# Performance work log

Hardware: AMD Instinct MI355X
Metric: run time of the kernel (lower is better)

## Reference

```python
import jax, jax.numpy as jnp
import numpy as np

STRIDES = (8, 16, 32)
IMG = 608
NC = 80
A = 3
IGNORE = 0.5
ANCHORS = np.array([[12, 16], [19, 36], [40, 28], [36, 75], [76, 55], [72, 146],
                    [142, 110], [192, 243], [459, 401]], np.float32)
ANCH_MASKS = ((0, 1, 2), (3, 4, 5), (6, 7, 8))
B, NL, NVALID = 16, 60, 45


def setup_inputs():
    key = jax.random.key(0)
    ks = jax.random.split(key, 8)
    inp = {}
    for i, s in enumerate(STRIDES):
        f = IMG // s
        inp[f"xin{i}"] = jax.random.normal(ks[i], (B, A * (5 + NC), f, f), jnp.float32)
    cx = jax.random.uniform(ks[3], (B, NL), minval=40.0, maxval=568.0)
    cy = jax.random.uniform(ks[4], (B, NL), minval=40.0, maxval=568.0)
    w = jax.random.uniform(ks[5], (B, NL), minval=8.0, maxval=120.0)
    h = jax.random.uniform(ks[6], (B, NL), minval=8.0, maxval=120.0)
    cls = jax.random.randint(ks[7], (B, NL), 0, NC).astype(jnp.float32)
    labels = jnp.stack([cx - w / 2, cy - h / 2, cx + w / 2, cy + h / 2, cls], -1)
    mask = (jnp.arange(NL) < NVALID)[None, :, None]
    inp["labels"] = jnp.where(mask, labels, 0.0)
    return inp


def _iou_cxcywh(p, t):  # p:[M,4] cx,cy,w,h; t:[N,4] -> [M,N]
    tl = jnp.maximum(p[:, None, :2] - p[:, None, 2:] / 2, t[None, :, :2] - t[None, :, 2:] / 2)
    br = jnp.minimum(p[:, None, :2] + p[:, None, 2:] / 2, t[None, :, :2] + t[None, :, 2:] / 2)
    ap = p[:, 2] * p[:, 3]
    at = t[:, 2] * t[:, 3]
    en = jnp.all(tl < br, -1)
    ai = jnp.prod(br - tl, -1) * en
    return ai / (ap[:, None] + at[None, :] - ai)


def _bce(p, t, w=None):
    # torch F.binary_cross_entropy with log clamped; clamp p instead (grad-safe, value-identical here)
    lp = jnp.log(jnp.maximum(p, 1e-12))
    l1p = jnp.log1p(-jnp.minimum(p, 1.0 - 1e-7))
    l = -(t * lp + (1.0 - t) * l1p)
    if w is not None:
        l = l * w
    return l.sum()


def _scale_loss(raw, labels, sid):
    stride = STRIDES[sid]
    f = IMG // stride
    n_ch = 5 + NC
    all_g = ANCHORS / stride  # [9,2] anchors in grid units
    m_anch = jnp.asarray(all_g[list(ANCH_MASKS[sid])])  # [3,2]
    b = raw.shape[0]
    out = raw.reshape(b, A, n_ch, f, f).transpose(0, 1, 3, 4, 2)  # [B,A,f,f,n_ch]
    xy = jax.nn.sigmoid(out[..., :2])
    wh = out[..., 2:4]
    obj = jax.nn.sigmoid(out[..., 4])
    clsp = jax.nn.sigmoid(out[..., 5:])

    gx = jnp.arange(f, dtype=jnp.float32)
    pred = jnp.stack([xy[..., 0] + gx[None, None, None, :],
                      xy[..., 1] + gx[None, None, :, None],
                      jnp.exp(wh[..., 0]) * m_anch[:, 0][None, :, None, None],
                      jnp.exp(wh[..., 1]) * m_anch[:, 1][None, :, None, None]], -1)

    valid = labels.sum(2) > 0  # [B,N]
    tx = (labels[..., 0] + labels[..., 2]) / (2 * stride)
    ty = (labels[..., 1] + labels[..., 3]) / (2 * stride)
    tw = (labels[..., 2] - labels[..., 0]) / stride
    th = (labels[..., 3] - labels[..., 1]) / stride
    ii = tx.astype(jnp.int32)
    jj = ty.astype(jnp.int32)

    # anchor-target IoU: both boxes anchored at origin -> closed form
    rw = jnp.asarray(all_g[:, 0])
    rh = jnp.asarray(all_g[:, 1])
    mw = jnp.minimum(tw[..., None], rw)
    mh = jnp.minimum(th[..., None], rh)
    inter = mw * mh * ((mw > 0) & (mh > 0))
    aiou = inter / (tw[..., None] * th[..., None] + rw * rh - inter)  # [B,N,9]
    best_all = jnp.argmax(aiou, -1)
    best_n = best_all % 3
    use = valid & (best_all // 3 == sid)

    # ignore mask from pred-vs-truth IoU
    tbox = jnp.stack([tx, ty, tw, th], -1)  # [B,N,4]
    ious = jax.vmap(_iou_cxcywh)(pred.reshape(b, -1, 4), tbox)  # [B,A*f*f,N]
    ious = ious * valid[:, None, :]
    obj_mask = (ious.max(-1).reshape(b, A, f, f) <= IGNORE).astype(jnp.float32)

    bb = jnp.broadcast_to(jnp.arange(b)[:, None], (b, labels.shape[1])).ravel()
    aa = best_n.ravel()
    jjs = jnp.where(use, jj, f).ravel()  # out-of-bounds index -> update dropped
    iis = ii.ravel()

    def scat(v):
        return jnp.zeros((b, A, f, f), jnp.float32).at[bb, aa, jjs, iis].set(v.ravel(), mode='drop')

    t0 = scat(tx - ii.astype(jnp.float32))
    t1 = scat(ty - jj.astype(jnp.float32))
    t2 = scat(jnp.log(tw / m_anch[best_n, 0] + 1e-16))
    t3 = scat(jnp.log(th / m_anch[best_n, 1] + 1e-16))
    t4 = scat(jnp.ones_like(tx))
    m = scat(jnp.ones_like(tx))
    sc = scat(jnp.sqrt(2.0 - tw * th / (f * f)))
    tcls = jnp.zeros((b, A, f, f, NC), jnp.float32).at[
        bb, aa, jjs, iis, labels[..., 4].astype(jnp.int32).ravel()].set(1.0, mode='drop')
    obj_mask = obj_mask.at[bb, aa, jjs, iis].set(1.0, mode='drop')

    m1 = m[..., None]
    sc1 = sc[..., None]
    o_xy = xy * m1
    g_xy = jnp.stack([t0, t1], -1) * m1
    o_wh = wh * m1 * sc1
    g_wh = jnp.stack([t2, t3], -1) * m1 * sc1
    o_ob = obj * obj_mask
    g_ob = t4 * obj_mask
    o_cl = clsp * m1
    g_cl = tcls * m1

    l_xy = _bce(o_xy, g_xy, (sc * sc)[..., None])
    l_wh = 0.5 * jnp.sum((o_wh - g_wh) ** 2)
    l_ob = _bce(o_ob, g_ob)
    l_cl = _bce(o_cl, g_cl)
    fo = jnp.concatenate([o_xy, o_wh, o_ob[..., None], o_cl], -1)
    ft = jnp.concatenate([g_xy, g_wh, g_ob[..., None], g_cl], -1)
    l2 = jnp.sum((fo - ft) ** 2)
    return jnp.stack([l_xy, l_wh, l_ob, l_cl, l2])


def reference(xin0, xin1, xin2, labels):
    parts = (_scale_loss(xin0, labels, 0) + _scale_loss(xin1, labels, 1)
             + _scale_loss(xin2, labels, 2))
    l_xy, l_wh, l_ob, l_cl, l2 = parts
    return jnp.stack([l_xy + l_wh + l_ob + l_cl, l_xy, l_wh, l_ob, l_cl, l2])
```

## Files before the change

### kernel.cpp

```cpp
#include <hip/hip_runtime.h>

#define BB 16
#define NL 60
#define NA 3
#define NC 80

#define NBX0C 17
#define NBX1C 5
#define NBX2C 2
#define NBXC  (NBX0C+NBX1C+NBX2C)
#define NBX   (NBXC+3)
#define NBLKT (NBX*BB)

__device__ __constant__ float d_AW[9] = {12.f,19.f,40.f,36.f,76.f,72.f,142.f,192.f,459.f};
__device__ __constant__ float d_AH[9] = {16.f,36.f,28.f,75.f,55.f,146.f,110.f,243.f,401.f};

__device__ __forceinline__ float sig_pos(float v){ return __fdividef(1.0f, 1.0f + __expf(-v)); }
__device__ __forceinline__ float sig_neg(float v){ return __fdividef(1.0f, 1.0f + __expf(v)); }
__device__ __forceinline__ float bcef(float p, float t){
    float lp  = __logf(fmaxf(p, 1e-12f));
    float l1p = __logf(1.0f - fminf(p, 1.0f - 1e-7f));
    return -(t*lp + (1.0f - t)*l1p);
}

template<int SID>
__device__ __forceinline__ bool cell_load(const float* __restrict__ raw, int xoff, int b, int tid,
        int &a, int &rembase, int &nc,
        float (&cx)[4], float (&cy)[4], float (&cw)[4], float (&ch)[4], float (&co)[4])
{
    constexpr int F  = (SID==0)?76:(SID==1)?38:19;
    constexpr int FF = F*F;
    int t = xoff*256 + tid;
    if (SID < 2){
        constexpr int NT = 3*FF/4;
        if (t >= NT) return false;
        a = t / (FF/4);
        rembase = 4*t - a*FF;
        nc = 4;
        const float* base = raw + ((size_t)(b*(NA*85) + a*85))*FF + rembase;
        float4 q0 = *reinterpret_cast<const float4*>(base);
        float4 q1 = *reinterpret_cast<const float4*>(base +   (size_t)FF);
        float4 q2 = *reinterpret_cast<const float4*>(base + 2*(size_t)FF);
        float4 q3 = *reinterpret_cast<const float4*>(base + 3*(size_t)FF);
        float4 q4 = *reinterpret_cast<const float4*>(base + 4*(size_t)FF);
        cx[0]=q0.x; cx[1]=q0.y; cx[2]=q0.z; cx[3]=q0.w;
        cy[0]=q1.x; cy[1]=q1.y; cy[2]=q1.z; cy[3]=q1.w;
        cw[0]=q2.x; cw[1]=q2.y; cw[2]=q2.z; cw[3]=q2.w;
        ch[0]=q3.x; ch[1]=q3.y; ch[2]=q3.z; ch[3]=q3.w;
        co[0]=q4.x; co[1]=q4.y; co[2]=q4.z; co[3]=q4.w;
    } else {
        constexpr int GPA = (FF+3)/4;
        if (t >= 3*GPA) return false;
        a = t / GPA;
        int k = t - a*GPA;
        rembase = 4*k;
        nc = (FF - rembase < 4) ? (FF - rembase) : 4;
        const float* base = raw + ((size_t)(b*(NA*85) + a*85))*FF + rembase;
        #pragma unroll
        for (int c=0;c<4;c++){
            bool v = c < nc;
            cx[c] = v ? base[c]              : 0.f;
            cy[c] = v ? base[(size_t)FF+c]   : 0.f;
            cw[c] = v ? base[2*(size_t)FF+c] : 0.f;
            ch[c] = v ? base[3*(size_t)FF+c] : 0.f;
            co[c] = v ? base[4*(size_t)FF+c] : 0.f;
        }
    }
    return true;
}

template<int SID>
__device__ __forceinline__ void cell_compute(int a, int rembase, int nc,
        const float (&cx)[4], const float (&cy)[4], const float (&cw)[4],
        const float (&ch)[4], const float (&co)[4],
        const float4* s_bx, const float* s_at3, const int* s_used, int nuse,
        float &lob, float &l2)
{
    constexpr int   F   = (SID==0)?76:(SID==1)?38:19;
    constexpr int   FF  = F*F;
    constexpr float RST = (SID==0)?0.125f:(SID==1)?0.0625f:0.03125f;
    float aw = d_AW[SID*3+a]*RST, ah = d_AH[SID*3+a]*RST;
    float plox[4],phix[4],ploy[4],phiy[4],apthr[4],lobv[4],l2v[4];
    int cellid[4];
    #pragma unroll
    for (int c=0;c<4;c++){
        int cel = rembase + c;
        int j = cel / F;
        int i = cel - j*F;
        float x = sig_pos(cx[c]), y = sig_pos(cy[c]);
        float pw = __expf(cw[c])*aw, ph = __expf(ch[c])*ah;
        float px = x + (float)i, py = y + (float)j;
        float hx = 0.5f*pw, hy = 0.5f*ph;
        plox[c]=px-hx; phix[c]=px+hx; ploy[c]=py-hy; phiy[c]=py+hy;
        apthr[c]=pw*ph*(1.0f/3.0f);
        float snb = sig_neg(co[c]);
        lobv[c] = -__logf(fmaxf(snb,1e-7f));
        float ob = 1.0f - snb;
        l2v[c] = ob*ob;
        cellid[c] = a*FF + cel;
    }
    bool skip0=false, skip1=false, skip2=false, skip3=false;
    #pragma unroll 2
    for (int l=0;l<NL;l++){
        float4 bb = s_bx[l];
        float thr = s_at3[l];
        float iw0 = fminf(phix[0],bb.y)-fmaxf(plox[0],bb.x);
        float ih0 = fminf(phiy[0],bb.w)-fmaxf(ploy[0],bb.z);
        float iw1 = fminf(phix[1],bb.y)-fmaxf(plox[1],bb.x);
        float ih1 = fminf(phiy[1],bb.w)-fmaxf(ploy[1],bb.z);
        float iw2 = fminf(phix[2],bb.y)-fmaxf(plox[2],bb.x);
        float ih2 = fminf(phiy[2],bb.w)-fmaxf(ploy[2],bb.z);
        float iw3 = fminf(phix[3],bb.y)-fmaxf(plox[3],bb.x);
        float ih3 = fminf(phiy[3],bb.w)-fmaxf(ploy[3],bb.z);
        skip0 = skip0 || (fmaxf(iw0,0.f)*fmaxf(ih0,0.f) > apthr[0]+thr);
        skip1 = skip1 || (fmaxf(iw1,0.f)*fmaxf(ih1,0.f) > apthr[1]+thr);
        skip2 = skip2 || (fmaxf(iw2,0.f)*fmaxf(ih2,0.f) > apthr[2]+thr);
        skip3 = skip3 || (fmaxf(iw3,0.f)*fmaxf(ih3,0.f) > apthr[3]+thr);
    }
    for (int k=0;k<nuse;k++){
        int uc = s_used[k];
        skip0 = skip0 || (uc==cellid[0]);
        skip1 = skip1 || (uc==cellid[1]);
        skip2 = skip2 || (uc==cellid[2]);
        skip3 = skip3 || (uc==cellid[3]);
    }
    if (0 < nc && !skip0){ lob += lobv[0]; l2 += l2v[0]; }
    if (1 < nc && !skip1){ lob += lobv[1]; l2 += l2v[1]; }
    if (2 < nc && !skip2){ lob += lobv[2]; l2 += l2v[2]; }
    if (3 < nc && !skip3){ lob += lobv[3]; l2 += l2v[3]; }
}

template<int SID>
__device__ __forceinline__ void target_pass(const float* __restrict__ raw, int b, int tid,
        const int* s_code, const float (*s_tv)[5],
        float &lxy, float &lwh, float &lob, float &lcl, float &l2)
{
    constexpr int F  = (SID==0)?76:(SID==1)?38:19;
    constexpr int FF = F*F;
    const int wv = tid>>6, lane = tid&63;
    int mycode = (lane < NL) ? s_code[lane] : -1;
    for (int l=wv; l<NL; l+=4){
        int cd = s_code[l];
        if (cd < 0) continue;
        int tcell = cd & 0xFFFFF;
        bool match = (mycode >= 0) && ((mycode & 0xFFFFF) == tcell);
        unsigned long long mask = __ballot(match);
        int last = 63 - __clzll(mask);
        if (last != l) continue;
        unsigned long long cm0=0ull, cm1=0ull, mm=mask;
        while (mm){
            int q = __ffsll((unsigned long long)mm) - 1;
            mm &= mm - 1;
            int cc = s_code[q] >> 20;
            if (cc < 64) cm0 |= 1ull<<cc; else cm1 |= 1ull<<(cc-64);
        }
        int aa = tcell / FF, rr = tcell - aa*FF;
        const float* cb = raw + ((size_t)(b*(NA*85) + aa*85))*FF + rr;
        float p1l = cb[(size_t)(5+lane)*FF];
        float p2l = (lane < 16) ? cb[(size_t)(69+lane)*FF] : 0.f;
        float e0=0.f,e1=0.f,e2=0.f,e3=0.f,e4=0.f;
        if (lane == 0){ e0=cb[0]; e1=cb[(size_t)FF]; e2=cb[2*(size_t)FF];
                        e3=cb[3*(size_t)FF]; e4=cb[4*(size_t)FF]; }
        float p1 = sig_pos(p1l);
        float t1v = (((cm0>>lane)&1ull)!=0ull) ? 1.f : 0.f;
        lcl += bcef(p1, t1v);
        float d1 = p1 - t1v; l2 += d1*d1;
        if (lane < 16){
            float p2 = sig_pos(p2l);
            float t2v = (((cm1>>lane)&1ull)!=0ull) ? 1.f : 0.f;
            lcl += bcef(p2, t2v);
            float d2 = p2 - t2v; l2 += d2*d2;
        }
        if (lane == 0){
            float xx=sig_pos(e0), yy=sig_pos(e1), ob=sig_pos(e4);
            float t0=s_tv[l][0], t1=s_tv[l][1], t2=s_tv[l][2], t3=s_tv[l][3], sc=s_tv[l][4];
            lxy += sc*sc*(bcef(xx,t0)+bcef(yy,t1));
            float d0=(e2-t2)*sc, dd=(e3-t3)*sc;
            lwh += 0.5f*(d0*d0+dd*dd);
            lob += -__logf(fmaxf(ob,1e-12f));
            float dx=xx-t0, dy=yy-t1, dob=ob-1.f;
            l2  += dx*dx+dy*dy+d0*d0+dd*dd+dob*dob;
        }
    }
}

__global__ __launch_bounds__(256) void fused_kernel(
        const float* __restrict__ x0, const float* __restrict__ x1,
        const float* __restrict__ x2, const float* __restrict__ labels,
        float* __restrict__ part)
{
    __shared__ float4 s_bx[NL];
    __shared__ float  s_at3[NL];
    __shared__ int    s_code[NL];
    __shared__ float  s_tv[NL][5];
    __shared__ int    s_used[NL];
    __shared__ int    s_nuse;
    __shared__ float  red[5][4];

    const int tid = threadIdx.x;
    const int bxi = blockIdx.x;
    const int b   = blockIdx.y;

    int sid, xoff, tgtblk;
    if      (bxi < NBX0C)       { sid = 0; xoff = bxi;               tgtblk = 0; }
    else if (bxi < NBX0C+NBX1C) { sid = 1; xoff = bxi-NBX0C;         tgtblk = 0; }
    else if (bxi < NBXC)        { sid = 2; xoff = bxi-(NBX0C+NBX1C); tgtblk = 0; }
    else                        { sid = bxi-NBXC; xoff = 0;          tgtblk = 1; }

    const float RSTv = (sid==0)?0.125f:(sid==1)?0.0625f:0.03125f;
    const int   F    = (sid==0)?76:(sid==1)?38:19;
    const int   FF   = F*F;
    const float* raw = (sid==0)?x0:(sid==1)?x1:x2;

    float cx[4],cy[4],cw[4],chn[4],co[4];
    int a=0, rembase=0, nc=0;
    bool active=false;
    if (!tgtblk){
        if      (sid==0) active = cell_load<0>(raw,xoff,b,tid,a,rembase,nc,cx,cy,cw,chn,co);
        else if (sid==1) active = cell_load<1>(raw,xoff,b,tid,a,rembase,nc,cx,cy,cw,chn,co);
        else             active = cell_load<2>(raw,xoff,b,tid,a,rembase,nc,cx,cy,cw,chn,co);
    }

    if (tid == 0) s_nuse = 0;
    __syncthreads();

    if (tid < NL){
        const float* lb = labels + ((size_t)b*NL + tid)*5;
        float x1f=lb[0], y1f=lb[1], x2f=lb[2], y2f=lb[3], cl=lb[4];
        bool valid = (x1f+y1f+x2f+y2f+cl) > 0.0f;
        float tx=(x1f+x2f)*0.5f*RSTv, ty=(y1f+y2f)*0.5f*RSTv;
        float tw=(x2f-x1f)*RSTv, th=(y2f-y1f)*RSTv;
        float at=tw*th;
        float best=-1.0f; int bi=0;
        #pragma unroll
        for (int k=0;k<9;k++){
            float rw=d_AW[k]*RSTv, rh=d_AH[k]*RSTv;
            float mw=fminf(tw,rw), mh=fminf(th,rh);
            float inter=(mw>0.f && mh>0.f)? mw*mh : 0.f;
            float aiou = inter/(at + rw*rh - inter);
            if (aiou > best){ best=aiou; bi=k; }
        }
        int bn = bi%3;
        bool use = valid && (bi/3 == sid);
        int ii=(int)tx, jj=(int)ty;
        float htw=0.5f*tw, hth=0.5f*th;
        s_bx[tid]  = make_float4(tx-htw, tx+htw, ty-hth, ty+hth);
        s_at3[tid] = at*(1.0f/3.0f);
        int cc = (bn*F + jj)*F + ii;
        s_code[tid] = use ? (cc | (((int)cl)<<20)) : -1;
        float aw=d_AW[sid*3+bn]*RSTv, ah=d_AH[sid*3+bn]*RSTv;
        s_tv[tid][0]=tx-(float)ii;
        s_tv[tid][1]=ty-(float)jj;
        s_tv[tid][2]=__logf(__fdividef(tw,aw) + 1e-16f);
        s_tv[tid][3]=__logf(__fdividef(th,ah) + 1e-16f);
        s_tv[tid][4]=sqrtf(2.0f - at/(float)FF);
        if (use){
            int p = atomicAdd(&s_nuse, 1);
            s_used[p] = cc;
        }
    }
    __syncthreads();

    float lxy=0.f, lwh=0.f, lob=0.f, lcl=0.f, l2=0.f;

    if (!tgtblk){
        if (active){
            int nuse = s_nuse;
            if      (sid==0) cell_compute<0>(a,rembase,nc,cx,cy,cw,chn,co,s_bx,s_at3,s_used,nuse,lob,l2);
            else if (sid==1) cell_compute<1>(a,rembase,nc,cx,cy,cw,chn,co,s_bx,s_at3,s_used,nuse,lob,l2);
            else             cell_compute<2>(a,rembase,nc,cx,cy,cw,chn,co,s_bx,s_at3,s_used,nuse,lob,l2);
        }
    } else {
        if      (sid==0) target_pass<0>(raw,b,tid,s_code,s_tv,lxy,lwh,lob,lcl,l2);
        else if (sid==1) target_pass<1>(raw,b,tid,s_code,s_tv,lxy,lwh,lob,lcl,l2);
        else             target_pass<2>(raw,b,tid,s_code,s_tv,lxy,lwh,lob,lcl,l2);
    }

    float v0=lxy, v1=lwh, v2=lob, v3=lcl, v4=l2;
    #pragma unroll
    for (int off=32; off>0; off>>=1){
        v0 += __shfl_down(v0, off, 64);
        v1 += __shfl_down(v1, off, 64);
        v2 += __shfl_down(v2, off, 64);
        v3 += __shfl_down(v3, off, 64);
        v4 += __shfl_down(v4, off, 64);
    }
    if ((tid & 63) == 0){
        int w = tid >> 6;
        red[0][w]=v0; red[1][w]=v1; red[2][w]=v2; red[3][w]=v3; red[4][w]=v4;
    }
    __syncthreads();
    if (tid == 0){
        int slot = b*NBX + bxi;
        #pragma unroll
        for (int c=0; c<5; c++){
            part[c*NBLKT + slot] = red[c][0]+red[c][1]+red[c][2]+red[c][3];
        }
    }
}

__global__ __launch_bounds__(256) void fin_kernel(const float* __restrict__ part,
                                                  float* __restrict__ out)
{
    __shared__ double red[5][4];
    int tid = threadIdx.x;
    double v[5] = {0,0,0,0,0};
    for (int i = tid; i < NBLKT; i += 256){
        #pragma unroll
        for (int c=0; c<5; c++) v[c] += (double)part[c*NBLKT + i];
    }
    #pragma unroll
    for (int off=32; off>0; off>>=1){
        #pragma unroll
        for (int c=0; c<5; c++) v[c] += __shfl_down(v[c], off, 64);
    }
    if ((tid & 63) == 0){
        int w = tid >> 6;
        #pragma unroll
        for (int c=0; c<5; c++) red[c][w] = v[c];
    }
    __syncthreads();
    if (tid == 0){
        double lxy = red[0][0]+red[0][1]+red[0][2]+red[0][3];
        double lwh = red[1][0]+red[1][1]+red[1][2]+red[1][3];
        double lob = red[2][0]+red[2][1]+red[2][2]+red[2][3];
        double lcl = red[3][0]+red[3][1]+red[3][2]+red[3][3];
        double l2  = red[4][0]+red[4][1]+red[4][2]+red[4][3];
        out[0]=(float)(lxy+lwh+lob+lcl);
        out[1]=(float)lxy; out[2]=(float)lwh; out[3]=(float)lob;
        out[4]=(float)lcl; out[5]=(float)l2;
    }
}

extern "C" void kernel_launch(void* const* d_in, const int* in_sizes, int n_in,
                              void* d_out, int out_size, void* d_ws, size_t ws_size,
                              hipStream_t stream) {
    const float* x0     = (const float*)d_in[0];
    const float* x1     = (const float*)d_in[1];
    const float* x2     = (const float*)d_in[2];
    const float* labels = (const float*)d_in[3];
    float* out = (float*)d_out;

    float* part = (float*)d_ws;

    fused_kernel<<<dim3(NBX, BB), 256, 0, stream>>>(x0, x1, x2, labels, part);
    fin_kernel<<<1, 256, 0, stream>>>(part, out);
}
```

Before: 27.29 us.

## Fuse final reduction via atomics and compact valid label boxes

Replaces the separate finalize kernel with per-block float atomic accumulation and a last-block-done counter that writes the outputs, adding a memset launch to zero the workspace. It also compacts valid label boxes into shared memory so the per-cell IoU loop only iterates over valid labels rather than all 60. Objectness sigmoid/log work is deferred until after the skip test so it is computed only for unskipped cells. Risks include float-atomic nondeterminism and loss of the double-precision final sum.

```diff
diff --git a/kernel.cpp b/kernel.cpp
--- a/kernel.cpp
+++ b/kernel.cpp
@@ -10,7 +10,9 @@
 #define NBX2C 2
 #define NBXC  (NBX0C+NBX1C+NBX2C)
 #define NBX   (NBXC+3)
-#define NBLKT (NBX*BB)
+#define TOTAL_BLOCKS (NBX*BB)
+
+#define SLOT_STRIDE 64
 
 __device__ __constant__ float d_AW[9] = {12.f,19.f,40.f,36.f,76.f,72.f,142.f,192.f,459.f};
 __device__ __constant__ float d_AH[9] = {16.f,36.f,28.f,75.f,55.f,146.f,110.f,243.f,401.f};
@@ -73,15 +75,15 @@
 __device__ __forceinline__ void cell_compute(int a, int rembase, int nc,
         const float (&cx)[4], const float (&cy)[4], const float (&cw)[4],
         const float (&ch)[4], const float (&co)[4],
-        const float4* s_bx, const float* s_at3, const int* s_used, int nuse,
+        const float4* s_bxc, const float* s_at3c, int nbx,
+        const int* s_used, int nuse,
         float &lob, float &l2)
 {
     constexpr int   F   = (SID==0)?76:(SID==1)?38:19;
     constexpr int   FF  = F*F;
     constexpr float RST = (SID==0)?0.125f:(SID==1)?0.0625f:0.03125f;
     float aw = d_AW[SID*3+a]*RST, ah = d_AH[SID*3+a]*RST;
-    float plox[4],phix[4],ploy[4],phiy[4],apthr[4],lobv[4],l2v[4];
-    int cellid[4];
+    float plox[4],phix[4],ploy[4],phiy[4],ap3[4];
     #pragma unroll
     for (int c=0;c<4;c++){
         int cel = rembase + c;
@@ -92,18 +94,13 @@
         float px = x + (float)i, py = y + (float)j;
         float hx = 0.5f*pw, hy = 0.5f*ph;
         plox[c]=px-hx; phix[c]=px+hx; ploy[c]=py-hy; phiy[c]=py+hy;
-        apthr[c]=pw*ph*(1.0f/3.0f);
-        float snb = sig_neg(co[c]);
-        lobv[c] = -__logf(fmaxf(snb,1e-7f));
-        float ob = 1.0f - snb;
-        l2v[c] = ob*ob;
-        cellid[c] = a*FF + cel;
+        ap3[c]=pw*ph*(1.0f/3.0f);
     }
     bool skip0=false, skip1=false, skip2=false, skip3=false;
     #pragma unroll 2
-    for (int l=0;l<NL;l++){
-        float4 bb = s_bx[l];
-        float thr = s_at3[l];
+    for (int l=0;l<nbx;l++){
+        float4 bb = s_bxc[l];
+        float thr = s_at3c[l];
         float iw0 = fminf(phix[0],bb.y)-fmaxf(plox[0],bb.x);
         float ih0 = fminf(phiy[0],bb.w)-fmaxf(ploy[0],bb.z);
         float iw1 = fminf(phix[1],bb.y)-fmaxf(plox[1],bb.x);
@@ -112,22 +109,29 @@
         float ih2 = fminf(phiy[2],bb.w)-fmaxf(ploy[2],bb.z);
         float iw3 = fminf(phix[3],bb.y)-fmaxf(plox[3],bb.x);
         float ih3 = fminf(phiy[3],bb.w)-fmaxf(ploy[3],bb.z);
-        skip0 = skip0 || (fmaxf(iw0,0.f)*fmaxf(ih0,0.f) > apthr[0]+thr);
-        skip1 = skip1 || (fmaxf(iw1,0.f)*fmaxf(ih1,0.f) > apthr[1]+thr);
-        skip2 = skip2 || (fmaxf(iw2,0.f)*fmaxf(ih2,0.f) > apthr[2]+thr);
-        skip3 = skip3 || (fmaxf(iw3,0.f)*fmaxf(ih3,0.f) > apthr[3]+thr);
-    }
+        skip0 = skip0 || (fmaxf(iw0,0.f)*fmaxf(ih0,0.f) > ap3[0]+thr);
+        skip1 = skip1 || (fmaxf(iw1,0.f)*fmaxf(ih1,0.f) > ap3[1]+thr);
+        skip2 = skip2 || (fmaxf(iw2,0.f)*fmaxf(ih2,0.f) > ap3[2]+thr);
+        skip3 = skip3 || (fmaxf(iw3,0.f)*fmaxf(ih3,0.f) > ap3[3]+thr);
+    }
+    int cellbase = a*FF + rembase;
     for (int k=0;k<nuse;k++){
         int uc = s_used[k];
-        skip0 = skip0 || (uc==cellid[0]);
-        skip1 = skip1 || (uc==cellid[1]);
-        skip2 = skip2 || (uc==cellid[2]);
-        skip3 = skip3 || (uc==cellid[3]);
-    }
-    if (0 < nc && !skip0){ lob += lobv[0]; l2 += l2v[0]; }
-    if (1 < nc && !skip1){ lob += lobv[1]; l2 += l2v[1]; }
-    if (2 < nc && !skip2){ lob += lobv[2]; l2 += l2v[2]; }
-    if (3 < nc && !skip3){ lob += lobv[3]; l2 += l2v[3]; }
+        skip0 = skip0 || (uc==cellbase);
+        skip1 = skip1 || (uc==cellbase+1);
+        skip2 = skip2 || (uc==cellbase+2);
+        skip3 = skip3 || (uc==cellbase+3);
+    }
+    #pragma unroll
+    for (int c=0;c<4;c++){
+        bool sk = (c==0)?skip0:(c==1)?skip1:(c==2)?skip2:skip3;
+        if (c < nc && !sk){
+            float snb = sig_neg(co[c]);
+            lob += -__logf(fmaxf(snb,1e-7f));
+            float ob = 1.0f - snb;
+            l2 += ob*ob;
+        }
+    }
 }
 
 template<int SID>
@@ -187,14 +191,15 @@
 __global__ __launch_bounds__(256) void fused_kernel(
         const float* __restrict__ x0, const float* __restrict__ x1,
         const float* __restrict__ x2, const float* __restrict__ labels,
-        float* __restrict__ part)
+        float* __restrict__ acc, unsigned* __restrict__ cnt,
+        float* __restrict__ out)
 {
-    __shared__ float4 s_bx[NL];
-    __shared__ float  s_at3[NL];
+    __shared__ float4 s_bxc[NL];
+    __shared__ float  s_at3c[NL];
     __shared__ int    s_code[NL];
     __shared__ float  s_tv[NL][5];
     __shared__ int    s_used[NL];
-    __shared__ int    s_nuse;
+    __shared__ int    s_nuse, s_nbx;
     __shared__ float  red[5][4];
 
     const int tid = threadIdx.x;
@@ -221,7 +226,7 @@
         else             active = cell_load<2>(raw,xoff,b,tid,a,rembase,nc,cx,cy,cw,chn,co);
     }
 
-    if (tid == 0) s_nuse = 0;
+    if (tid == 0){ s_nuse = 0; s_nbx = 0; }
     __syncthreads();
 
     if (tid < NL){
@@ -243,9 +248,6 @@
         int bn = bi%3;
         bool use = valid && (bi/3 == sid);
         int ii=(int)tx, jj=(int)ty;
-        float htw=0.5f*tw, hth=0.5f*th;
-        s_bx[tid]  = make_float4(tx-htw, tx+htw, ty-hth, ty+hth);
-        s_at3[tid] = at*(1.0f/3.0f);
         int cc = (bn*F + jj)*F + ii;
         s_code[tid] = use ? (cc | (((int)cl)<<20)) : -1;
         float aw=d_AW[sid*3+bn]*RSTv, ah=d_AH[sid*3+bn]*RSTv;
@@ -254,6 +256,12 @@
         s_tv[tid][2]=__logf(__fdividef(tw,aw) + 1e-16f);
         s_tv[tid][3]=__logf(__fdividef(th,ah) + 1e-16f);
         s_tv[tid][4]=sqrtf(2.0f - at/(float)FF);
+        if (valid){
+            int p = atomicAdd(&s_nbx, 1);
+            float htw=0.5f*tw, hth=0.5f*th;
+            s_bxc[p]  = make_float4(tx-htw, tx+htw, ty-hth, ty+hth);
+            s_at3c[p] = at*(1.0f/3.0f);
+        }
         if (use){
             int p = atomicAdd(&s_nuse, 1);
             s_used[p] = cc;
@@ -265,10 +273,10 @@
 
     if (!tgtblk){
         if (active){
-            int nuse = s_nuse;
-            if      (sid==0) cell_compute<0>(a,rembase,nc,cx,cy,cw,chn,co,s_bx,s_at3,s_used,nuse,lob,l2);
-            else if (sid==1) cell_compute<1>(a,rembase,nc,cx,cy,cw,chn,co,s_bx,s_at3,s_used,nuse,lob,l2);
-            else             cell_compute<2>(a,rembase,nc,cx,cy,cw,chn,co,s_bx,s_at3,s_used,nuse,lob,l2);
+            int nuse = s_nuse, nbx = s_nbx;
+            if      (sid==0) cell_compute<0>(a,rembase,nc,cx,cy,cw,chn,co,s_bxc,s_at3c,nbx,s_used,nuse,lob,l2);
+            else if (sid==1) cell_compute<1>(a,rembase,nc,cx,cy,cw,chn,co,s_bxc,s_at3c,nbx,s_used,nuse,lob,l2);
+            else             cell_compute<2>(a,rembase,nc,cx,cy,cw,chn,co,s_bxc,s_at3c,nbx,s_used,nuse,lob,l2);
         }
     } else {
         if      (sid==0) target_pass<0>(raw,b,tid,s_code,s_tv,lxy,lwh,lob,lcl,l2);
@@ -291,44 +299,27 @@
     }
     __syncthreads();
     if (tid == 0){
-        int slot = b*NBX + bxi;
-        #pragma unroll
-        for (int c=0; c<5; c++){
-            part[c*NBLKT + slot] = red[c][0]+red[c][1]+red[c][2]+red[c][3];
-        }
-    }
-}
-
-__global__ __launch_bounds__(256) void fin_kernel(const float* __restrict__ part,
-                                                  float* __restrict__ out)
-{
-    __shared__ double red[5][4];
-    int tid = threadIdx.x;
-    double v[5] = {0,0,0,0,0};
-    for (int i = tid; i < NBLKT; i += 256){
-        #pragma unroll
-        for (int c=0; c<5; c++) v[c] += (double)part[c*NBLKT + i];
-    }
-    #pragma unroll
-    for (int off=32; off>0; off>>=1){
-        #pragma unroll
-        for (int c=0; c<5; c++) v[c] += __shfl_down(v[c], off, 64);
-    }
-    if ((tid & 63) == 0){
-        int w = tid >> 6;
-        #pragma unroll
-        for (int c=0; c<5; c++) red[c][w] = v[c];
-    }
-    __syncthreads();
-    if (tid == 0){
-        double lxy = red[0][0]+red[0][1]+red[0][2]+red[0][3];
-        double lwh = red[1][0]+red[1][1]+red[1][2]+red[1][3];
-        double lob = red[2][0]+red[2][1]+red[2][2]+red[2][3];
-        double lcl = red[3][0]+red[3][1]+red[3][2]+red[3][3];
-        double l2  = red[4][0]+red[4][1]+red[4][2]+red[4][3];
-        out[0]=(float)(lxy+lwh+lob+lcl);
-        out[1]=(float)lxy; out[2]=(float)lwh; out[3]=(float)lob;
-        out[4]=(float)lcl; out[5]=(float)l2;
+        float c0 = red[0][0]+red[0][1]+red[0][2]+red[0][3];
+        float c1 = red[1][0]+red[1][1]+red[1][2]+red[1][3];
+        float c2 = red[2][0]+red[2][1]+red[2][2]+red[2][3];
+        float c3 = red[3][0]+red[3][1]+red[3][2]+red[3][3];
+        float c4 = red[4][0]+red[4][1]+red[4][2]+red[4][3];
+        atomicAdd(&acc[0*SLOT_STRIDE], c0);
+        atomicAdd(&acc[1*SLOT_STRIDE], c1);
+        atomicAdd(&acc[2*SLOT_STRIDE], c2);
+        atomicAdd(&acc[3*SLOT_STRIDE], c3);
+        atomicAdd(&acc[4*SLOT_STRIDE], c4);
+        __threadfence();
+        unsigned old = atomicAdd(cnt, 1u);
+        if (old == TOTAL_BLOCKS-1){
+            float t1 = atomicExch(&acc[0*SLOT_STRIDE], 0.f);
+            float t2 = atomicExch(&acc[1*SLOT_STRIDE], 0.f);
+            float t3 = atomicExch(&acc[2*SLOT_STRIDE], 0.f);
+            float t4 = atomicExch(&acc[3*SLOT_STRIDE], 0.f);
+            float t5 = atomicExch(&acc[4*SLOT_STRIDE], 0.f);
+            out[0]=t1+t2+t3+t4;
+            out[1]=t1; out[2]=t2; out[3]=t3; out[4]=t4; out[5]=t5;
+        }
     }
 }
 
@@ -341,8 +332,10 @@
     const float* labels = (const float*)d_in[3];
     float* out = (float*)d_out;
 
-    float* part = (float*)d_ws;
-
-    fused_kernel<<<dim3(NBX, BB), 256, 0, stream>>>(x0, x1, x2, labels, part);
-    fin_kernel<<<1, 256, 0, stream>>>(part, out);
-}
+    float*    acc = (float*)d_ws;
+    unsigned* cnt = (unsigned*)((char*)d_ws + 5*256);
+
+    hipMemsetAsync(d_ws, 0, 6*256, stream);
+
+    fused_kernel<<<dim3(NBX, BB), 256, 0, stream>>>(x0, x1, x2, labels, acc, cnt, out);
+}
```

Result: slower. 31.68 us (+16.1%).
